# Performance work log

Hardware: AMD Instinct MI355X
Metric: run time of the kernel (lower is better)

## Reference

```python
import jax, jax.numpy as jnp
import numpy as np

HEADS = 4
DIM_HEAD = 64


def setup_inputs() -> dict:
    key = jax.random.key(0)
    k1, k2, k3, k4 = jax.random.split(key, 4)
    dim = 256
    hidden = HEADS * DIM_HEAD  # 256
    x = jax.random.normal(k1, (16, dim, 64, 64), dtype=jnp.float32)
    # 1x1 conv weights stored as [out_c, in_c]
    w_qkv = jax.random.normal(k2, (3 * hidden, dim), dtype=jnp.float32) * (1.0 / np.sqrt(dim))
    w_out = jax.random.normal(k3, (dim, hidden), dtype=jnp.float32) * (1.0 / np.sqrt(hidden))
    b_out = jax.random.normal(k4, (dim,), dtype=jnp.float32) * 0.01
    gamma = jnp.ones((dim,), dtype=jnp.float32) * 1e-05
    return {"x": x, "w_qkv": w_qkv, "w_out": w_out, "b_out": b_out, "gamma": gamma}


def reference(x, w_qkv, w_out, b_out, gamma):
    b, c, h, w = x.shape
    n = h * w
    # 1x1 conv == channel matmul
    qkv = jnp.einsum('oc,bchw->bohw', w_qkv, x)  # [b, 3*heads*dh, h, w]
    qkv = qkv.reshape(b, 3, HEADS, DIM_HEAD, n)  # channel split order: (qkv, heads, c)
    q, k, v = qkv[:, 0], qkv[:, 1], qkv[:, 2]    # each [b, heads, dh, n]
    k = jax.nn.softmax(k, axis=-1)               # softmax over spatial tokens
    context = jnp.einsum('bhdn,bhen->bhde', k, v)  # [b, heads, dh, dh]
    out = jnp.einsum('bhde,bhdn->bhen', context, q)  # [b, heads, dh, n]
    out = out.reshape(b, HEADS * DIM_HEAD, h, w)
    y = jnp.einsum('oc,bchw->bohw', w_out, out) + b_out[None, :, None, None]
    return y * gamma[None, :, None, None] + x
```

## Files before the change

### kernel.cpp

```cpp
#include <hip/hip_runtime.h>
#include <stdint.h>

typedef short s16x8 __attribute__((ext_vector_type(8)));
typedef float f32x4 __attribute__((ext_vector_type(4)));
typedef unsigned int u32x2 __attribute__((ext_vector_type(2)));

typedef const __attribute__((address_space(1))) void glb_cv;
typedef __attribute__((address_space(3))) void lds_v;

__device__ __forceinline__ float bits2f(unsigned short u) {
    union { unsigned int i; float f; } c; c.i = ((unsigned int)u) << 16; return c.f;
}
__device__ __forceinline__ unsigned short f2bits(float f) {
    union { float f; unsigned int i; } c; c.f = f;
    unsigned int x = c.i;
    unsigned int r = (x + 0x7FFFu + ((x >> 16) & 1u)) >> 16;
    return (unsigned short)r;
}
__device__ __forceinline__ unsigned int pack2(float a, float b) {
    return (unsigned int)f2bits(a) | ((unsigned int)f2bits(b) << 16);
}

__device__ __forceinline__ void gl_lds16(const void* g, void* l) {
    __builtin_amdgcn_global_load_lds((glb_cv*)g, (lds_v*)l, 16, 0, 0);
}

__global__ __launch_bounds__(256) void k_cvt(
    const float* __restrict__ src, unsigned short* __restrict__ dst, int n8)
{
    int i = blockIdx.x * 256 + threadIdx.x;
    if (i >= n8) return;
    const float* s = src + (size_t)i * 8;
    float4 a = *(const float4*)s, b = *(const float4*)(s + 4);
    unsigned int q[4] = { pack2(a.x, a.y), pack2(a.z, a.w), pack2(b.x, b.y), pack2(b.z, b.w) };
    *(s16x8*)(dst + (size_t)i * 8) = *(s16x8*)q;
}

__global__ __launch_bounds__(256) void k_transpose(
    const unsigned short* __restrict__ src, unsigned short* __restrict__ dst,
    int RS, int DS)
{
    int dr = blockIdx.x * 256 + threadIdx.x;
    int c0 = blockIdx.y * 8;
    __align__(16) unsigned short tmp[8];
#pragma unroll
    for (int j = 0; j < 8; ++j) tmp[j] = src[(size_t)(c0 + j) * RS + dr];
    *(s16x8*)(dst + (size_t)dr * DS + c0) = *(s16x8*)tmp;
}

__global__ __launch_bounds__(256) void k_prepw(
    const float* __restrict__ wqkv, const float* __restrict__ wout,
    unsigned short* __restrict__ wb, unsigned short* __restrict__ wob,
    unsigned short* __restrict__ WqT)
{
    int i = blockIdx.x * 256 + threadIdx.x;
    if (i < 32768) {
        const float* s; unsigned short* d; int j;
        if (i < 24576) { s = wqkv; d = wb; j = i; }
        else           { s = wout; d = wob; j = i - 24576; }
        const float* sp = s + (size_t)j * 8;
        float4 a = *(const float4*)sp, b = *(const float4*)(sp + 4);
        unsigned int q[4] = { pack2(a.x, a.y), pack2(a.z, a.w), pack2(b.x, b.y), pack2(b.z, b.w) };
        *(s16x8*)(d + (size_t)j * 8) = *(s16x8*)q;
    } else {
        int j = i - 32768;
        int dr = j & 255, c0 = (j >> 8) * 8;
        __align__(16) unsigned short tmp[8];
#pragma unroll
        for (int jj = 0; jj < 8; ++jj)
            tmp[jj] = f2bits(wqkv[(size_t)(c0 + jj) * 256 + dr]);
        *(s16x8*)(WqT + (size_t)dr * 256 + c0) = *(s16x8*)tmp;
    }
}

__global__ __launch_bounds__(256) void k_prep(
    const float* __restrict__ x, unsigned short* __restrict__ xT,
    unsigned short* __restrict__ xbf)
{
    __shared__ unsigned short Ts[64][264];
    int b = blockIdx.y, n0 = blockIdx.x * 64, t = threadIdx.x;
    const float* xb = x + (size_t)b * 1048576;
    unsigned short* xbfb = xbf + (size_t)b * 1048576;
#pragma unroll
    for (int i = 0; i < 16; ++i) {
        int idx = t + i * 256;
        int c = idx >> 4, nq = idx & 15;
        float4 v = *(const float4*)(xb + (size_t)c * 4096 + n0 + nq * 4);
        u32x2 q; q[0] = pack2(v.x, v.y); q[1] = pack2(v.z, v.w);
        *(u32x2*)(xbfb + (size_t)c * 4096 + n0 + nq * 4) = q;
        float vv[4] = { v.x, v.y, v.z, v.w };
#pragma unroll
        for (int e = 0; e < 4; ++e) {
            int ee = (e + c) & 3;
            Ts[nq * 4 + ee][c] = f2bits(vv[ee]);
        }
    }
    __syncthreads();
    unsigned short* xTb = xT + (size_t)b * 1048576 + (size_t)n0 * 256;
#pragma unroll
    for (int i = 0; i < 8; ++i) {
        int idx = t + i * 256;
        int nl = idx >> 5, cg = (idx & 31) * 8;
        *(s16x8*)(xTb + (size_t)nl * 256 + cg) = *(const s16x8*)&Ts[nl][cg];
    }
}

template <int EPI>
__global__ __launch_bounds__(256) void gemm_bt2(
    const unsigned short* __restrict__ A, const unsigned short* __restrict__ Bt,
    void* __restrict__ C,
    int K, int Kstep, int lda, int ldb, int ldc,
    long Abs, long Bbs, long Cbs,
    const float* __restrict__ Xres,
    const float* __restrict__ gamma,
    const float* __restrict__ bias)
{
    __shared__ __align__(16) unsigned short As[128 * 64];
    __shared__ __align__(16) unsigned short Bs[128 * 64];
    int bz = blockIdx.z;
    int b = bz & 15, kc = bz >> 4;
    int m0 = blockIdx.y * 128, n0 = blockIdx.x * 128;
    const unsigned short* Ab = A + (size_t)b * Abs + (size_t)m0 * lda + (size_t)kc * Kstep;
    const unsigned short* Bb = Bt + (size_t)b * Bbs + (size_t)n0 * ldb + (size_t)kc * Kstep;
    int t = threadIdx.x;
    int w = t >> 6, l = t & 63, lm = l & 15, lq = l >> 4;
    int mw = (w >> 1) * 64, nw = (w & 1) * 64;

    f32x4 acc[4][4];
    f32x4 zero = {0.f, 0.f, 0.f, 0.f};
#pragma unroll
    for (int i = 0; i < 4; ++i)
#pragma unroll
        for (int j = 0; j < 4; ++j) acc[i][j] = zero;

    for (int kk = 0; kk < K; kk += 64) {
#pragma unroll
        for (int i = 0; i < 4; ++i) {
            int idx = t + i * 256;
            int r = idx >> 3;
            int sch = (idx & 7) ^ (r & 7);
            int lbase = (i * 256 + w * 64) * 8;
            gl_lds16(Ab + (size_t)r * lda + kk + sch * 8, &As[lbase]);
            gl_lds16(Bb + (size_t)r * ldb + kk + sch * 8, &Bs[lbase]);
        }
        __syncthreads();
#pragma unroll
        for (int ks = 0; ks < 2; ++ks) {
            s16x8 af[4], bfr[4];
#pragma unroll
            for (int mi = 0; mi < 4; ++mi) {
                int row = mw + mi * 16 + lm;
                af[mi] = *(const s16x8*)&As[row * 64 + (((ks * 4 + lq) ^ (row & 7)) << 3)];
            }
#pragma unroll
            for (int ni = 0; ni < 4; ++ni) {
                int row = nw + ni * 16 + lm;
                bfr[ni] = *(const s16x8*)&Bs[row * 64 + (((ks * 4 + lq) ^ (row & 7)) << 3)];
            }
#pragma unroll
            for (int mi = 0; mi < 4; ++mi)
#pragma unroll
                for (int ni = 0; ni < 4; ++ni)
                    acc[mi][ni] = __builtin_amdgcn_mfma_f32_16x16x32_bf16(af[mi], bfr[ni], acc[mi][ni], 0, 0, 0);
        }
        __syncthreads();
    }

    if (EPI == 0) {
        unsigned short* Cb = (unsigned short*)C + (size_t)bz * Cbs;
#pragma unroll
        for (int mi = 0; mi < 4; ++mi)
#pragma unroll
            for (int r = 0; r < 4; ++r) {
                int m = m0 + mw + mi * 16 + lq * 4 + r;
#pragma unroll
                for (int ni = 0; ni < 4; ++ni) {
                    int n = n0 + nw + ni * 16 + lm;
                    Cb[(size_t)m * ldc + n] = f2bits(acc[mi][ni][r]);
                }
            }
    } else {
        float* Cb = (float*)C + (size_t)bz * Cbs;
        const float* Xb = Xres + (size_t)bz * Cbs;
#pragma unroll
        for (int mi = 0; mi < 4; ++mi)
#pragma unroll
            for (int r = 0; r < 4; ++r) {
                int m = m0 + mw + mi * 16 + lq * 4 + r;
                float g = gamma[m], bo = bias[m];
#pragma unroll
                for (int ni = 0; ni < 4; ++ni) {
                    int n = n0 + nw + ni * 16 + lm;
                    size_t idx = (size_t)m * ldc + n;
                    Cb[idx] = g * (acc[mi][ni][r] + bo) + Xb[idx];
                }
            }
    }
}

__global__ __launch_bounds__(256) void gemm64(
    const unsigned short* __restrict__ A, const unsigned short* __restrict__ Bt,
    unsigned short* __restrict__ C,
    int K, int Kstep, int lda, int ldb, int ldc,
    long Abs, long Bbs, long Cbs)
{
    __shared__ __align__(16) unsigned short As[64 * 64];
    __shared__ __align__(16) unsigned short Bs[64 * 64];
    int bz = blockIdx.z;
    int b = bz & 15, kc = bz >> 4;
    int m0 = blockIdx.y * 64, n0 = blockIdx.x * 64;
    const unsigned short* Ab = A + (size_t)b * Abs + (size_t)m0 * lda + (size_t)kc * Kstep;
    const unsigned short* Bb = Bt + (size_t)b * Bbs + (size_t)n0 * ldb + (size_t)kc * Kstep;
    int t = threadIdx.x;
    int w = t >> 6, l = t & 63, lm = l & 15, lq = l >> 4;
    int mw = (w >> 1) * 32, nw = (w & 1) * 32;

    f32x4 acc[2][2];
    f32x4 zero = {0.f, 0.f, 0.f, 0.f};
#pragma unroll
    for (int i = 0; i < 2; ++i)
#pragma unroll
        for (int j = 0; j < 2; ++j) acc[i][j] = zero;

    for (int kk = 0; kk < K; kk += 64) {
#pragma unroll
        for (int i = 0; i < 2; ++i) {
            int idx = t + i * 256;
            int r = idx >> 3;
            int sch = (idx & 7) ^ (r & 7);
            int lbase = (i * 256 + w * 64) * 8;
            gl_lds16(Ab + (size_t)r * lda + kk + sch * 8, &As[lbase]);
            gl_lds16(Bb + (size_t)r * ldb + kk + sch * 8, &Bs[lbase]);
        }
        __syncthreads();
#pragma unroll
        for (int ks = 0; ks < 2; ++ks) {
            s16x8 af[2], bfr[2];
#pragma unroll
            for (int mi = 0; mi < 2; ++mi) {
                int row = mw + mi * 16 + lm;
                af[mi] = *(const s16x8*)&As[row * 64 + (((ks * 4 + lq) ^ (row & 7)) << 3)];
            }
#pragma unroll
            for (int ni = 0; ni < 2; ++ni) {
                int row = nw + ni * 16 + lm;
                bfr[ni] = *(const s16x8*)&Bs[row * 64 + (((ks * 4 + lq) ^ (row & 7)) << 3)];
            }
#pragma unroll
            for (int mi = 0; mi < 2; ++mi)
#pragma unroll
                for (int ni = 0; ni < 2; ++ni)
                    acc[mi][ni] = __builtin_amdgcn_mfma_f32_16x16x32_bf16(af[mi], bfr[ni], acc[mi][ni], 0, 0, 0);
        }
        __syncthreads();
    }

    unsigned short* Cb = C + (size_t)bz * Cbs;
#pragma unroll
    for (int mi = 0; mi < 2; ++mi)
#pragma unroll
        for (int r = 0; r < 4; ++r) {
            int m = m0 + mw + mi * 16 + lq * 4 + r;
#pragma unroll
            for (int ni = 0; ni < 2; ++ni) {
                int n = n0 + nw + ni * 16 + lm;
                Cb[(size_t)m * ldc + n] = f2bits(acc[mi][ni][r]);
            }
        }
}

template <int BF32, int EPI>
__global__ __launch_bounds__(256) void gemm_bt(
    const unsigned short* __restrict__ A, const void* __restrict__ Bt,
    void* __restrict__ C,
    int K, int Kstep, int lda, int ldb, int ldc,
    long Abs, long Bbs, long Cbs,
    const float* __restrict__ Xres,
    const float* __restrict__ gamma,
    const float* __restrict__ bias)
{
    __shared__ unsigned short As[128][72];
    __shared__ unsigned short Bs[128][72];
    int bz = blockIdx.z;
    int b = bz & 15, kc = bz >> 4;
    int m0 = blockIdx.y * 128, n0 = blockIdx.x * 128;
    const unsigned short* Ab = A + (size_t)b * Abs + (size_t)m0 * lda + (size_t)kc * Kstep;
    size_t boff = (size_t)b * Bbs + (size_t)n0 * ldb + (size_t)kc * Kstep;
    int t = threadIdx.x;
    int w = t >> 6, l = t & 63, lm = l & 15, lq = l >> 4;
    int mw = (w >> 1) * 64, nw = (w & 1) * 64;

    f32x4 acc[4][4];
    f32x4 zero = {0.f, 0.f, 0.f, 0.f};
#pragma unroll
    for (int i = 0; i < 4; ++i)
#pragma unroll
        for (int j = 0; j < 4; ++j) acc[i][j] = zero;

    for (int kk = 0; kk < K; kk += 64) {
#pragma unroll
        for (int i = 0; i < 4; ++i) {
            int idx = t + i * 256;
            int r = idx >> 3, ch = idx & 7;
            *(s16x8*)&As[r][ch * 8] = *(const s16x8*)(Ab + (size_t)r * lda + kk + ch * 8);
            if (BF32) {
                const float* bp = (const float*)Bt + boff + (size_t)r * ldb + kk + ch * 8;
                float4 v0 = *(const float4*)bp, v1 = *(const float4*)(bp + 4);
                unsigned int q[4] = { pack2(v0.x, v0.y), pack2(v0.z, v0.w),
                                      pack2(v1.x, v1.y), pack2(v1.z, v1.w) };
                *(s16x8*)&Bs[r][ch * 8] = *(s16x8*)q;
            } else {
                const unsigned short* bp = (const unsigned short*)Bt + boff + (size_t)r * ldb + kk + ch * 8;
                *(s16x8*)&Bs[r][ch * 8] = *(const s16x8*)bp;
            }
        }
        __syncthreads();
#pragma unroll
        for (int ks = 0; ks < 2; ++ks) {
            s16x8 af[4], bfr[4];
#pragma unroll
            for (int mi = 0; mi < 4; ++mi) af[mi]  = *(const s16x8*)&As[mw + mi * 16 + lm][ks * 32 + lq * 8];
#pragma unroll
            for (int ni = 0; ni < 4; ++ni) bfr[ni] = *(const s16x8*)&Bs[nw + ni * 16 + lm][ks * 32 + lq * 8];
#pragma unroll
            for (int mi = 0; mi < 4; ++mi)
#pragma unroll
                for (int ni = 0; ni < 4; ++ni)
                    acc[mi][ni] = __builtin_amdgcn_mfma_f32_16x16x32_bf16(af[mi], bfr[ni], acc[mi][ni], 0, 0, 0);
        }
        __syncthreads();
    }

    if (EPI == 0) {
        unsigned short* Cb = (unsigned short*)C + (size_t)bz * Cbs;
#pragma unroll
        for (int mi = 0; mi < 4; ++mi)
#pragma unroll
            for (int r = 0; r < 4; ++r) {
                int m = m0 + mw + mi * 16 + lq * 4 + r;
#pragma unroll
                for (int ni = 0; ni < 4; ++ni) {
                    int n = n0 + nw + ni * 16 + lm;
                    Cb[(size_t)m * ldc + n] = f2bits(acc[mi][ni][r]);
                }
            }
    } else {
        float* Cb = (float*)C + (size_t)bz * Cbs;
        const float* Xb = Xres + (size_t)bz * Cbs;
#pragma unroll
        for (int mi = 0; mi < 4; ++mi)
#pragma unroll
            for (int r = 0; r < 4; ++r) {
                int m = m0 + mw + mi * 16 + lq * 4 + r;
                float g = gamma[m], bo = bias[m];
#pragma unroll
                for (int ni = 0; ni < 4; ++ni) {
                    int n = n0 + nw + ni * 16 + lm;
                    size_t idx = (size_t)m * ldc + n;
                    Cb[idx] = g * (acc[mi][ni][r] + bo) + Xb[idx];
                }
            }
    }
}

template <int EPI>
__global__ __launch_bounds__(256) void gemm_bn(
    const unsigned short* __restrict__ A, const float* __restrict__ B,
    void* __restrict__ C,
    int K, int lda, int ldb, int ldc,
    long Abs, long Bbs, long Cbs,
    const float* __restrict__ Xres,
    const float* __restrict__ gamma,
    const float* __restrict__ bias)
{
    __shared__ unsigned short As[128][72];
    __shared__ unsigned short Bs[64][130];
    int bz = blockIdx.z;
    int m0 = blockIdx.y * 128, n0 = blockIdx.x * 128;
    const unsigned short* Ab = A + (size_t)bz * Abs + (size_t)m0 * lda;
    const float* Bb = B + (size_t)bz * Bbs + n0;
    int t = threadIdx.x;
    int w = t >> 6, l = t & 63, lm = l & 15, lq = l >> 4;
    int mw = (w >> 1) * 64, nw = (w & 1) * 64;

    f32x4 acc[4][4];
    f32x4 zero = {0.f, 0.f, 0.f, 0.f};
#pragma unroll
    for (int i = 0; i < 4; ++i)
#pragma unroll
        for (int j = 0; j < 4; ++j) acc[i][j] = zero;

    for (int kk = 0; kk < K; kk += 64) {
#pragma unroll
        for (int i = 0; i < 4; ++i) {
            int idx = t + i * 256;
            int r = idx >> 3, ch = idx & 7;
            *(s16x8*)&As[r][ch * 8] = *(const s16x8*)(Ab + (size_t)r * lda + kk + ch * 8);
        }
#pragma unroll
        for (int i = 0; i < 4; ++i) {
            int idx = t + i * 256;
            int c = idx >> 4, cc = idx & 15;
            const float* bp = Bb + (size_t)(kk + c) * ldb + cc * 8;
            float4 v0 = *(const float4*)bp, v1 = *(const float4*)(bp + 4);
            unsigned int* q = (unsigned int*)&Bs[c][cc * 8];
            q[0] = pack2(v0.x, v0.y); q[1] = pack2(v0.z, v0.w);
            q[2] = pack2(v1.x, v1.y); q[3] = pack2(v1.z, v1.w);
        }
        __syncthreads();
#pragma unroll
        for (int ks = 0; ks < 2; ++ks) {
            s16x8 af[4];
#pragma unroll
            for (int mi = 0; mi < 4; ++mi) af[mi] = *(const s16x8*)&As[mw + mi * 16 + lm][ks * 32 + lq * 8];
#pragma unroll
            for (int ni = 0; ni < 4; ++ni) {
                s16x8 bfr;
#pragma unroll
                for (int j = 0; j < 8; ++j) bfr[j] = (short)Bs[ks * 32 + lq * 8 + j][nw + ni * 16 + lm];
#pragma unroll
                for (int mi = 0; mi < 4; ++mi)
                    acc[mi][ni] = __builtin_amdgcn_mfma_f32_16x16x32_bf16(af[mi], bfr, acc[mi][ni], 0, 0, 0);
            }
        }
        __syncthreads();
    }

#pragma unroll
    for (int mi = 0; mi < 4; ++mi)
#pragma unroll
        for (int r = 0; r < 4; ++r) {
            int m = m0 + mw + mi * 16 + lq * 4 + r;
            float g = 0.f, bo = 0.f;
            if (EPI == 1) { g = gamma[m]; bo = bias[m]; }
#pragma unroll
            for (int ni = 0; ni < 4; ++ni) {
                int n = n0 + nw + ni * 16 + lm;
                size_t idx = (size_t)m * ldc + n;
                float v = acc[mi][ni][r];
                if (EPI == 1) {
                    float* Cb = (float*)C + (size_t)bz * Cbs;
                    Cb[idx] = g * (v + bo) + Xres[(size_t)bz * Cbs + idx];
                } else {
                    unsigned short* Cb = (unsigned short*)C + (size_t)bz * Cbs;
                    Cb[idx] = f2bits(v);
                }
            }
        }
}

__global__ __launch_bounds__(256) void k_softmax(unsigned short* __restrict__ kbuf)
{
    unsigned short* p = kbuf + (size_t)blockIdx.x * 4096;
    int t = threadIdx.x;
    __shared__ float red[4];

    s16x8 r0 = *(const s16x8*)(p + t * 16);
    s16x8 r1 = *(const s16x8*)(p + t * 16 + 8);
    float v[16];
    float m = -1e30f;
#pragma unroll
    for (int i = 0; i < 8; ++i) { v[i] = bits2f((unsigned short)r0[i]); v[8 + i] = bits2f((unsigned short)r1[i]); }
#pragma unroll
    for (int i = 0; i < 16; ++i) m = fmaxf(m, v[i]);
#pragma unroll
    for (int off = 32; off >= 1; off >>= 1) m = fmaxf(m, __shfl_xor(m, off));
    if ((t & 63) == 0) red[t >> 6] = m;
    __syncthreads();
    m = fmaxf(fmaxf(red[0], red[1]), fmaxf(red[2], red[3]));
    __syncthreads();

    float s = 0.f;
#pragma unroll
    for (int i = 0; i < 16; ++i) { v[i] = __expf(v[i] - m); s += v[i]; }
#pragma unroll
    for (int off = 32; off >= 1; off >>= 1) s += __shfl_xor(s, off);
    if ((t & 63) == 0) red[t >> 6] = s;
    __syncthreads();
    s = red[0] + red[1] + red[2] + red[3];
    float inv = 1.0f / s;

    __align__(16) unsigned short otmp[16];
#pragma unroll
    for (int i = 0; i < 16; ++i) otmp[i] = f2bits(v[i] * inv);
    *(s16x8*)(p + t * 16) = *(s16x8*)(otmp);
    *(s16x8*)(p + t * 16 + 8) = *(s16x8*)(otmp + 8);
}

template <int NC>
__global__ __launch_bounds__(256) void k_gred(
    const unsigned short* __restrict__ Gp, unsigned short* __restrict__ G)
{
    int gid = blockIdx.x * 256 + threadIdx.x;
    int b = gid >> 13;
    size_t i8 = (size_t)(gid & 8191) * 8;
    float s[8] = {0.f, 0.f, 0.f, 0.f, 0.f, 0.f, 0.f, 0.f};
#pragma unroll
    for (int kc = 0; kc < NC; ++kc) {
        s16x8 v = *(const s16x8*)(Gp + (size_t)(kc * 16 + b) * 65536 + i8);
#pragma unroll
        for (int j = 0; j < 8; ++j) s[j] += bits2f((unsigned short)v[j]);
    }
    __align__(16) unsigned short tmp[8];
#pragma unroll
    for (int j = 0; j < 8; ++j) tmp[j] = f2bits(s[j]);
    *(s16x8*)(G + (size_t)b * 65536 + i8) = *(s16x8*)tmp;
}

__global__ __launch_bounds__(256) void k_ctxw2(
    const unsigned short* __restrict__ G, const unsigned short* __restrict__ wb,
    const unsigned short* __restrict__ wob, unsigned short* __restrict__ W2)
{
    __shared__ unsigned short ctxs[64][72];
    int h = blockIdx.x, b = blockIdx.y;
    int t = threadIdx.x, w = t >> 6, l = t & 63, lm = l & 15, lq = l >> 4;
    const unsigned short* Gb = G + (size_t)b * 65536 + (size_t)(h * 64) * 256;
    const unsigned short* Wv = wb + 131072 + (size_t)(h * 64) * 256;
    f32x4 zero = {0.f, 0.f, 0.f, 0.f};

    f32x4 acc[4];
#pragma unroll
    for (int i = 0; i < 4; ++i) acc[i] = zero;
    for (int kk = 0; kk < 256; kk += 32) {
        s16x8 a = *(const s16x8*)(Gb + (size_t)(w * 16 + lm) * 256 + kk + lq * 8);
#pragma unroll
        for (int ni = 0; ni < 4; ++ni) {
            s16x8 bb = *(const s16x8*)(Wv + (size_t)(ni * 16 + lm) * 256 + kk + lq * 8);
            acc[ni] = __builtin_amdgcn_mfma_f32_16x16x32_bf16(a, bb, acc[ni], 0, 0, 0);
        }
    }
#pragma unroll
    for (int ni = 0; ni < 4; ++ni)
#pragma unroll
        for (int r = 0; r < 4; ++r)
            ctxs[w * 16 + lq * 4 + r][ni * 16 + lm] = f2bits(acc[ni][r]);
    __syncthreads();

    f32x4 acc2[4][4];
#pragma unroll
    for (int i = 0; i < 4; ++i)
#pragma unroll
        for (int j = 0; j < 4; ++j) acc2[i][j] = zero;
#pragma unroll
    for (int ks = 0; ks < 2; ++ks) {
        s16x8 af[4], bfr[4];
#pragma unroll
        for (int mi = 0; mi < 4; ++mi)
            af[mi] = *(const s16x8*)(wob + (size_t)(w * 64 + mi * 16 + lm) * 256 + h * 64 + ks * 32 + lq * 8);
#pragma unroll
        for (int ni = 0; ni < 4; ++ni) bfr[ni] = *(const s16x8*)&ctxs[ni * 16 + lm][ks * 32 + lq * 8];
#pragma unroll
        for (int mi = 0; mi < 4; ++mi)
#pragma unroll
            for (int ni = 0; ni < 4; ++ni)
                acc2[mi][ni] = __builtin_amdgcn_mfma_f32_16x16x32_bf16(af[mi], bfr[ni], acc2[mi][ni], 0, 0, 0);
    }
    unsigned short* W2b = W2 + (size_t)b * 65536;
#pragma unroll
    for (int mi = 0; mi < 4; ++mi)
#pragma unroll
        for (int r = 0; r < 4; ++r) {
            int o = w * 64 + mi * 16 + lq * 4 + r;
#pragma unroll
            for (int ni = 0; ni < 4; ++ni)
                W2b[(size_t)o * 256 + h * 64 + ni * 16 + lm] = f2bits(acc2[mi][ni][r]);
        }
}

extern "C" void kernel_launch(void* const* d_in, const int* in_sizes, int n_in,
                              void* d_out, int out_size, void* d_ws, size_t ws_size,
                              hipStream_t stream)
{
    (void)in_sizes; (void)n_in; (void)out_size;
    const float* x      = (const float*)d_in[0];
    const float* w_qkv  = (const float*)d_in[1];
    const float* w_out  = (const float*)d_in[2];
    const float* b_out  = (const float*)d_in[3];
    const float* gamma  = (const float*)d_in[4];

    char* ws = (char*)d_ws;
    const size_t NEED = 40501248;

    if (ws_size >= NEED) {
        unsigned short* xT  = (unsigned short*)ws;
        unsigned short* W3  = (unsigned short*)(ws + 33554432);
        unsigned short* Gp  = (unsigned short*)(ws + 35651584);
        unsigned short* WqT = (unsigned short*)(ws + 39845888);
        unsigned short* wb  = (unsigned short*)(ws + 39976960);
        unsigned short* wob = (unsigned short*)(ws + 40370176);
        unsigned short* kbuf = (unsigned short*)d_out;
        unsigned short* xbf  = (unsigned short*)d_out + 16777216;
        unsigned short* G    = (unsigned short*)d_out;
        unsigned short* W2   = (unsigned short*)d_out + 1048576;

        k_prepw<<<dim3(160), 256, 0, stream>>>(w_qkv, w_out, wb, wob, WqT);

        k_prep<<<dim3(64, 16), 256, 0, stream>>>(x, xT, xbf);

        gemm_bt2<0><<<dim3(32, 2, 16), 256, 0, stream>>>(
            wb + 65536, xT, kbuf, 256, 0, 256, 256, 4096,
            0L, 1048576L, 1048576L, nullptr, nullptr, nullptr);

        k_softmax<<<dim3(4096), 256, 0, stream>>>(kbuf);

        gemm64<<<dim3(4, 4, 32), 256, 0, stream>>>(
            kbuf, xbf, Gp, 2048, 2048, 4096, 4096, 256,
            1048576L, 1048576L, 65536L);

        k_gred<2><<<dim3(512), 256, 0, stream>>>(Gp, G);

        k_ctxw2<<<dim3(4, 16), 256, 0, stream>>>(G, wb, wob, W2);

        gemm64<<<dim3(4, 4, 16), 256, 0, stream>>>(
            W2, WqT, W3, 256, 0, 256, 256, 256,
            65536L, 0L, 65536L);

        gemm_bt2<1><<<dim3(32, 2, 16), 256, 0, stream>>>(
            W3, xT, d_out, 256, 0, 256, 256, 4096,
            65536L, 1048576L, 1048576L, x, gamma, b_out);
    } else {
        unsigned short* kbuf = (unsigned short*)d_out;
        unsigned short* Gp  = (unsigned short*)(ws);
        unsigned short* G   = (unsigned short*)(ws + 16777216);
        unsigned short* W2  = (unsigned short*)(ws + 18874368);
        unsigned short* W3  = (unsigned short*)(ws + 20971520);
        unsigned short* WqT = (unsigned short*)(ws + 23068672);
        unsigned short* wb  = (unsigned short*)(ws + 23199744);
        unsigned short* wob = (unsigned short*)(ws + 23592960);

        k_cvt<<<dim3(96), 256, 0, stream>>>(w_qkv, wb, 24576);
        k_cvt<<<dim3(32), 256, 0, stream>>>(w_out, wob, 8192);
        k_transpose<<<dim3(1, 32, 1), 256, 0, stream>>>(wb, WqT, 256, 256);

        gemm_bn<0><<<dim3(32, 2, 16), 256, 0, stream>>>(
            wb + 65536, x, kbuf, 256, 256, 4096, 4096,
            0L, 1048576L, 1048576L, nullptr, nullptr, nullptr);

        k_softmax<<<dim3(4096), 256, 0, stream>>>(kbuf);

        gemm_bt<1, 0><<<dim3(2, 2, 128), 256, 0, stream>>>(
            kbuf, x, Gp, 512, 512, 4096, 4096, 256,
            1048576L, 1048576L, 65536L, nullptr, nullptr, nullptr);

        k_gred<8><<<dim3(512), 256, 0, stream>>>(Gp, G);
        k_ctxw2<<<dim3(4, 16), 256, 0, stream>>>(G, wb, wob, W2);

        gemm_bt<0, 0><<<dim3(2, 2, 16), 256, 0, stream>>>(
            W2, WqT, W3, 256, 0, 256, 256, 256,
            65536L, 0L, 65536L, nullptr, nullptr, nullptr);

        gemm_bn<1><<<dim3(32, 2, 16), 256, 0, stream>>>(
            W3, x, d_out, 256, 256, 4096, 4096,
            65536L, 1048576L, 1048576L, x, gamma, b_out);
    }
}
```

Baseline: 230.0 us.

## Double-buffer LDS tiles in gemm_bt2 and gemm64 to overlap loads with MFMA

```diff
diff --git a/kernel.cpp b/kernel.cpp
--- a/kernel.cpp
+++ b/kernel.cpp
@@ -115,8 +115,8 @@
     const float* __restrict__ gamma,
     const float* __restrict__ bias)
 {
-    __shared__ __align__(16) unsigned short As[128 * 64];
-    __shared__ __align__(16) unsigned short Bs[128 * 64];
+    __shared__ __align__(16) unsigned short As[2][128 * 64];
+    __shared__ __align__(16) unsigned short Bs[2][128 * 64];
     int bz = blockIdx.z;
     int b = bz & 15, kc = bz >> 4;
     int m0 = blockIdx.y * 128, n0 = blockIdx.x * 128;
@@ -133,29 +133,30 @@
 #pragma unroll
         for (int j = 0; j < 4; ++j) acc[i][j] = zero;
 
-    for (int kk = 0; kk < K; kk += 64) {
+    auto stage = [&](int buf, int kk) {
 #pragma unroll
         for (int i = 0; i < 4; ++i) {
             int idx = t + i * 256;
             int r = idx >> 3;
             int sch = (idx & 7) ^ (r & 7);
             int lbase = (i * 256 + w * 64) * 8;
-            gl_lds16(Ab + (size_t)r * lda + kk + sch * 8, &As[lbase]);
-            gl_lds16(Bb + (size_t)r * ldb + kk + sch * 8, &Bs[lbase]);
-        }
-        __syncthreads();
+            gl_lds16(Ab + (size_t)r * lda + kk + sch * 8, &As[buf][lbase]);
+            gl_lds16(Bb + (size_t)r * ldb + kk + sch * 8, &Bs[buf][lbase]);
+        }
+    };
+    auto compute = [&](int buf) {
 #pragma unroll
         for (int ks = 0; ks < 2; ++ks) {
             s16x8 af[4], bfr[4];
 #pragma unroll
             for (int mi = 0; mi < 4; ++mi) {
                 int row = mw + mi * 16 + lm;
-                af[mi] = *(const s16x8*)&As[row * 64 + (((ks * 4 + lq) ^ (row & 7)) << 3)];
+                af[mi] = *(const s16x8*)&As[buf][row * 64 + (((ks * 4 + lq) ^ (row & 7)) << 3)];
             }
 #pragma unroll
             for (int ni = 0; ni < 4; ++ni) {
                 int row = nw + ni * 16 + lm;
-                bfr[ni] = *(const s16x8*)&Bs[row * 64 + (((ks * 4 + lq) ^ (row & 7)) << 3)];
+                bfr[ni] = *(const s16x8*)&Bs[buf][row * 64 + (((ks * 4 + lq) ^ (row & 7)) << 3)];
             }
 #pragma unroll
             for (int mi = 0; mi < 4; ++mi)
@@ -163,8 +164,23 @@
                 for (int ni = 0; ni < 4; ++ni)
                     acc[mi][ni] = __builtin_amdgcn_mfma_f32_16x16x32_bf16(af[mi], bfr[ni], acc[mi][ni], 0, 0, 0);
         }
-        __syncthreads();
-    }
+    };
+
+    stage(0, 0);
+    asm volatile("s_waitcnt vmcnt(0)" ::: "memory");
+    __builtin_amdgcn_s_barrier();
+    __builtin_amdgcn_sched_barrier(0);
+
+    int cur = 0;
+    for (int kk = 64; kk < K; kk += 64) {
+        stage(cur ^ 1, kk);
+        compute(cur);
+        asm volatile("s_waitcnt vmcnt(0)" ::: "memory");
+        __builtin_amdgcn_s_barrier();
+        __builtin_amdgcn_sched_barrier(0);
+        cur ^= 1;
+    }
+    compute(cur);
 
     if (EPI == 0) {
         unsigned short* Cb = (unsigned short*)C + (size_t)bz * Cbs;
@@ -204,8 +220,8 @@
     int K, int Kstep, int lda, int ldb, int ldc,
     long Abs, long Bbs, long Cbs)
 {
-    __shared__ __align__(16) unsigned short As[64 * 64];
-    __shared__ __align__(16) unsigned short Bs[64 * 64];
+    __shared__ __align__(16) unsigned short As[2][64 * 64];
+    __shared__ __align__(16) unsigned short Bs[2][64 * 64];
     int bz = blockIdx.z;
     int b = bz & 15, kc = bz >> 4;
     int m0 = blockIdx.y * 64, n0 = blockIdx.x * 64;
@@ -222,29 +238,30 @@
 #pragma unroll
         for (int j = 0; j < 2; ++j) acc[i][j] = zero;
 
-    for (int kk = 0; kk < K; kk += 64) {
+    auto stage = [&](int buf, int kk) {
 #pragma unroll
         for (int i = 0; i < 2; ++i) {
             int idx = t + i * 256;
             int r = idx >> 3;
             int sch = (idx & 7) ^ (r & 7);
             int lbase = (i * 256 + w * 64) * 8;
-            gl_lds16(Ab + (size_t)r * lda + kk + sch * 8, &As[lbase]);
-            gl_lds16(Bb + (size_t)r * ldb + kk + sch * 8, &Bs[lbase]);
-        }
-        __syncthreads();
+            gl_lds16(Ab + (size_t)r * lda + kk + sch * 8, &As[buf][lbase]);
+            gl_lds16(Bb + (size_t)r * ldb + kk + sch * 8, &Bs[buf][lbase]);
+        }
+    };
+    auto compute = [&](int buf) {
 #pragma unroll
         for (int ks = 0; ks < 2; ++ks) {
             s16x8 af[2], bfr[2];
 #pragma unroll
             for (int mi = 0; mi < 2; ++mi) {
                 int row = mw + mi * 16 + lm;
-                af[mi] = *(const s16x8*)&As[row * 64 + (((ks * 4 + lq) ^ (row & 7)) << 3)];
+                af[mi] = *(const s16x8*)&As[buf][row * 64 + (((ks * 4 + lq) ^ (row & 7)) << 3)];
             }
 #pragma unroll
             for (int ni = 0; ni < 2; ++ni) {
                 int row = nw + ni * 16 + lm;
-                bfr[ni] = *(const s16x8*)&Bs[row * 64 + (((ks * 4 + lq) ^ (row & 7)) << 3)];
+                bfr[ni] = *(const s16x8*)&Bs[buf][row * 64 + (((ks * 4 + lq) ^ (row & 7)) << 3)];
             }
 #pragma unroll
             for (int mi = 0; mi < 2; ++mi)
@@ -252,8 +269,23 @@
                 for (int ni = 0; ni < 2; ++ni)
                     acc[mi][ni] = __builtin_amdgcn_mfma_f32_16x16x32_bf16(af[mi], bfr[ni], acc[mi][ni], 0, 0, 0);
         }
-        __syncthreads();
-    }
+    };
+
+    stage(0, 0);
+    asm volatile("s_waitcnt vmcnt(0)" ::: "memory");
+    __builtin_amdgcn_s_barrier();
+    __builtin_amdgcn_sched_barrier(0);
+
+    int cur = 0;
+    for (int kk = 64; kk < K; kk += 64) {
+        stage(cur ^ 1, kk);
+        compute(cur);
+        asm volatile("s_waitcnt vmcnt(0)" ::: "memory");
+        __builtin_amdgcn_s_barrier();
+        __builtin_amdgcn_sched_barrier(0);
+        cur ^= 1;
+    }
+    compute(cur);
 
     unsigned short* Cb = C + (size_t)bz * Cbs;
 #pragma unroll
```

Result: no change. 229.5 us (-0.2%).
